# Performance work log

Measured on AMD Instinct MI355X. Metric: run time of the kernel, lower is better.

The kernel has to match this reference:

```python
import jax, jax.numpy as jnp
import numpy as np

D_MODEL = 1024
NUM_HEADS = 16
HEAD_DIM = D_MODEL // NUM_HEADS
SEQ_LEN = 4096
BATCH = 1
ROPE_THETA = 10000.0


def apply_rope(x, theta):
    # x: [B, H, S, D], interleaved pair rotation (x_{2i}, x_{2i+1})
    D = x.shape[-1]
    S = x.shape[-2]
    pos = jnp.arange(S, dtype=jnp.float32)
    inv_freq = theta ** (-jnp.arange(0, D, 2, dtype=jnp.float32) / D)  # [D/2]
    ang = pos[:, None] * inv_freq[None, :]  # [S, D/2]
    cos = jnp.cos(ang).astype(x.dtype)
    sin = jnp.sin(ang).astype(x.dtype)
    x1 = x[..., 0::2]
    x2 = x[..., 1::2]
    r1 = x1 * cos - x2 * sin
    r2 = x1 * sin + x2 * cos
    return jnp.stack([r1, r2], axis=-1).reshape(x.shape)


def setup_inputs() -> dict:
    key = jax.random.key(0)
    ks = jax.random.split(key, 5)
    s = 1.0 / np.sqrt(D_MODEL)
    return {
        "x": jax.random.normal(ks[0], (BATCH, SEQ_LEN, D_MODEL), jnp.float32),
        "Wq": jax.random.normal(ks[1], (D_MODEL, D_MODEL), jnp.float32) * s,
        "Wk": jax.random.normal(ks[2], (D_MODEL, D_MODEL), jnp.float32) * s,
        "Wv": jax.random.normal(ks[3], (D_MODEL, D_MODEL), jnp.float32) * s,
        "Wo": jax.random.normal(ks[4], (D_MODEL, D_MODEL), jnp.float32) * s,
    }


def reference(x, Wq, Wk, Wv, Wo):
    B, S, _ = x.shape
    # bias-free linear: y = x @ W.T
    def proj(W):
        y = jnp.einsum('bsd,ed->bse', x, W)
        return y.reshape(B, S, NUM_HEADS, HEAD_DIM).transpose(0, 2, 1, 3)  # [B,H,S,hd]
    q = apply_rope(proj(Wq), ROPE_THETA)
    k = apply_rope(proj(Wk), ROPE_THETA)
    v = proj(Wv)
    scale = 1.0 / jnp.sqrt(jnp.asarray(HEAD_DIM, dtype=x.dtype))
    scores = jnp.einsum('bhqd,bhkd->bhqk', q, k) * scale  # [B,H,S,S]
    causal = jnp.tril(jnp.ones((S, S), dtype=bool))
    scores = jnp.where(causal, scores, jnp.asarray(-jnp.inf, dtype=scores.dtype))
    attn = jax.nn.softmax(scores, axis=-1)
    out = jnp.einsum('bhqk,bhkd->bhqd', attn, v)
    out = out.transpose(0, 2, 1, 3).reshape(B, S, D_MODEL)
    return jnp.einsum('bsd,ed->bse', out, Wo)
```

## Files before the change

### kernel.cpp

```cpp
#include <hip/hip_runtime.h>
#include <math.h>

#define SEQ 4096
#define DM  1024
#define NH  16

typedef __attribute__((ext_vector_type(8))) short bf16x8;
typedef __attribute__((ext_vector_type(4))) float f32x4;
typedef __attribute__((ext_vector_type(16))) float f32x16;
typedef __attribute__((ext_vector_type(4))) unsigned int u32x4;

#define QSCALE 0.18033688011112042f
#define SMAX 16.0f

__device__ __forceinline__ unsigned short f2bf(float f){
  unsigned int u = __float_as_uint(f);
  u += 0x7fffu + ((u >> 16) & 1u);
  return (unsigned short)(u >> 16);
}

__device__ __forceinline__ unsigned int cvtpk(float lo, float hi){
  unsigned int r;
  asm("v_cvt_pk_bf16_f32 %0, %1, %2" : "=v"(r) : "v"(lo), "v"(hi));
  return r;
}

__device__ __forceinline__ void gload_lds16(const void* g, void* l){
  __builtin_amdgcn_global_load_lds(
      (const __attribute__((address_space(1))) unsigned int*)g,
      (__attribute__((address_space(3))) unsigned int*)l,
      16, 0, 0);
}

__global__ __launch_bounds__(256) void f2bf_kernel(const float* __restrict__ src,
                                                   unsigned short* __restrict__ dst, int n4){
  int i = blockIdx.x * 256 + threadIdx.x;
  int stride = gridDim.x * 256;
  for (; i < n4; i += stride){
    float4 v = ((const float4*)src)[i];
    ushort4 o; o.x = f2bf(v.x); o.y = f2bf(v.y); o.z = f2bf(v.z); o.w = f2bf(v.w);
    ((ushort4*)dst)[i] = o;
  }
}

__global__ __launch_bounds__(256) void wf2bf_kernel(const float* __restrict__ a, const float* __restrict__ b,
                                                    const float* __restrict__ c, const float* __restrict__ d,
                                                    unsigned short* __restrict__ oa, unsigned short* __restrict__ ob,
                                                    unsigned short* __restrict__ oc, unsigned short* __restrict__ od,
                                                    int n4){
  const int sel = blockIdx.y;
  const float* src = (sel == 0) ? a : (sel == 1) ? b : (sel == 2) ? c : d;
  unsigned short* dst = (sel == 0) ? oa : (sel == 1) ? ob : (sel == 2) ? oc : od;
  int i = blockIdx.x * 256 + threadIdx.x;
  int stride = gridDim.x * 256;
  for (; i < n4; i += stride){
    float4 v = ((const float4*)src)[i];
    ushort4 o; o.x = f2bf(v.x); o.y = f2bf(v.y); o.z = f2bf(v.z); o.w = f2bf(v.w);
    ((ushort4*)dst)[i] = o;
  }
}

__global__ __launch_bounds__(256) void rope_tab_kernel(float2* __restrict__ tab){
  int i = blockIdx.x * 256 + threadIdx.x;
  int s = i >> 5, f = i & 31;
  double inv = exp2(-(double)f * (13.287712379549449 / 32.0));
  double a = (double)s * inv;
  const double twopi = 6.283185307179586476;
  a -= twopi * floor(a / twopi);
  float af = (float)a;
  tab[i] = make_float2(cosf(af), sinf(af));
}

__global__ __launch_bounds__(256) void qkv_gemm(const unsigned short* __restrict__ A,
                                                const unsigned short* __restrict__ Wq,
                                                const unsigned short* __restrict__ Wk,
                                                const unsigned short* __restrict__ Wv,
                                                unsigned short* __restrict__ Qo,
                                                unsigned short* __restrict__ Ko,
                                                unsigned short* __restrict__ Vto,
                                                const float2* __restrict__ rope)
{
  __shared__ unsigned short At[128 * 32];
  __shared__ unsigned short Bt[128 * 32];
  const int sel = blockIdx.x >> 3;
  const unsigned short* B = (sel == 0) ? Wq : (sel == 1) ? Wk : Wv;
  const int K = DM;
  const int t = threadIdx.x;
  const int lane = t & 63, w = t >> 6;
  const int lg = lane >> 4, lr = lane & 15;
  const int wr = w >> 1, wc = w & 1;
  const int m0 = blockIdx.y * 128, n0 = (blockIdx.x & 7) * 128;

  f32x4 acc[4][4];
  #pragma unroll
  for (int mi = 0; mi < 4; mi++)
    #pragma unroll
    for (int nj = 0; nj < 4; nj++)
      acc[mi][nj] = (f32x4){0.f, 0.f, 0.f, 0.f};

  for (int k0 = 0; k0 < K; k0 += 32){
    __syncthreads();
    {
      int idx = t;
      gload_lds16(&A[(size_t)(m0 + (idx >> 2)) * K + k0 + (idx & 3) * 8], &At[idx * 8]);
      gload_lds16(&B[(size_t)(n0 + (idx >> 2)) * K + k0 + (idx & 3) * 8], &Bt[idx * 8]);
      idx = t + 256;
      gload_lds16(&A[(size_t)(m0 + (idx >> 2)) * K + k0 + (idx & 3) * 8], &At[idx * 8]);
      gload_lds16(&B[(size_t)(n0 + (idx >> 2)) * K + k0 + (idx & 3) * 8], &Bt[idx * 8]);
    }
    __syncthreads();
    bf16x8 af[4], bfr[4];
    #pragma unroll
    for (int mi = 0; mi < 4; mi++)
      af[mi] = *(const bf16x8*)&At[(wr * 64 + mi * 16 + lr) * 32 + lg * 8];
    #pragma unroll
    for (int nj = 0; nj < 4; nj++)
      bfr[nj] = *(const bf16x8*)&Bt[(wc * 64 + nj * 16 + lr) * 32 + lg * 8];
    #pragma unroll
    for (int mi = 0; mi < 4; mi++)
      #pragma unroll
      for (int nj = 0; nj < 4; nj++)
        acc[mi][nj] = __builtin_amdgcn_mfma_f32_16x16x32_bf16(af[mi], bfr[nj], acc[mi][nj], 0, 0, 0);
  }

  #pragma unroll
  for (int mi = 0; mi < 4; mi++){
    #pragma unroll
    for (int nj = 0; nj < 4; nj++){
      f32x4 v = acc[mi][nj];
      int col  = n0 + wc * 64 + nj * 16 + lr;
      int row0 = m0 + wr * 64 + mi * 16 + lg * 4;
      if (sel == 0){
        #pragma unroll
        for (int j = 0; j < 4; j++){
          float val = v[j];
          float oth = __shfl_xor(val, 1);
          int row = row0 + j;
          int i = (col & 63) >> 1;
          float2 cs = rope[row * 32 + i];
          float res = ((col & 1) == 0) ? (val * cs.x - oth * cs.y)
                                       : (oth * cs.y + val * cs.x);
          Qo[(size_t)row * DM + col] = f2bf(res * QSCALE);
        }
      } else if (sel == 1){
        const int hh = col >> 6, d = col & 63;
        #pragma unroll
        for (int j = 0; j < 4; j++){
          float val = v[j];
          float oth = __shfl_xor(val, 1);
          int row = row0 + j;
          int i = d >> 1;
          float2 cs = rope[row * 32 + i];
          float res = ((d & 1) == 0) ? (val * cs.x - oth * cs.y)
                                     : (oth * cs.y + val * cs.x);
          size_t idx = ((size_t)((hh * 128 + (row >> 5)) * 8 + (d >> 3))) * 256
                       + (row & 31) * 8 + (d & 7);
          Ko[idx] = f2bf(res);
        }
      } else {
        const int hh = col >> 6, d = col & 63;
        ushort4 pkv; pkv.x = f2bf(v[0]); pkv.y = f2bf(v[1]); pkv.z = f2bf(v[2]); pkv.w = f2bf(v[3]);
        size_t idx = ((size_t)(((hh * 2 + (d >> 5)) * 64 + (row0 >> 6)) * 8 + ((row0 >> 3) & 7))) * 256
                     + (d & 31) * 8 + (row0 & 7);
        *(ushort4*)&Vto[idx] = pkv;
      }
    }
  }
}

__global__ __launch_bounds__(256) void gemm_out(const unsigned short* __restrict__ A,
                                                const unsigned short* __restrict__ B,
                                                float* __restrict__ C)
{
  __shared__ unsigned short At[128 * 32];
  __shared__ unsigned short Bt[128 * 32];
  const int K = DM;
  const int t = threadIdx.x;
  const int lane = t & 63, w = t >> 6;
  const int lg = lane >> 4, lr = lane & 15;
  const int wr = w >> 1, wc = w & 1;
  const int m0 = blockIdx.y * 128, n0 = blockIdx.x * 128;

  f32x4 acc[4][4];
  #pragma unroll
  for (int mi = 0; mi < 4; mi++)
    #pragma unroll
    for (int nj = 0; nj < 4; nj++)
      acc[mi][nj] = (f32x4){0.f, 0.f, 0.f, 0.f};

  for (int k0 = 0; k0 < K; k0 += 32){
    __syncthreads();
    {
      int idx = t;
      gload_lds16(&A[(size_t)(m0 + (idx >> 2)) * K + k0 + (idx & 3) * 8], &At[idx * 8]);
      gload_lds16(&B[(size_t)(n0 + (idx >> 2)) * K + k0 + (idx & 3) * 8], &Bt[idx * 8]);
      idx = t + 256;
      gload_lds16(&A[(size_t)(m0 + (idx >> 2)) * K + k0 + (idx & 3) * 8], &At[idx * 8]);
      gload_lds16(&B[(size_t)(n0 + (idx >> 2)) * K + k0 + (idx & 3) * 8], &Bt[idx * 8]);
    }
    __syncthreads();
    bf16x8 af[4], bfr[4];
    #pragma unroll
    for (int mi = 0; mi < 4; mi++)
      af[mi] = *(const bf16x8*)&At[(wr * 64 + mi * 16 + lr) * 32 + lg * 8];
    #pragma unroll
    for (int nj = 0; nj < 4; nj++)
      bfr[nj] = *(const bf16x8*)&Bt[(wc * 64 + nj * 16 + lr) * 32 + lg * 8];
    #pragma unroll
    for (int mi = 0; mi < 4; mi++)
      #pragma unroll
      for (int nj = 0; nj < 4; nj++)
        acc[mi][nj] = __builtin_amdgcn_mfma_f32_16x16x32_bf16(af[mi], bfr[nj], acc[mi][nj], 0, 0, 0);
  }

  #pragma unroll
  for (int mi = 0; mi < 4; mi++)
    #pragma unroll
    for (int nj = 0; nj < 4; nj++){
      f32x4 v = acc[mi][nj];
      int col  = n0 + wc * 64 + nj * 16 + lr;
      int row0 = m0 + wr * 64 + mi * 16 + lg * 4;
      #pragma unroll
      for (int j = 0; j < 4; j++)
        C[(size_t)(row0 + j) * DM + col] = v[j];
    }
}

__global__ __launch_bounds__(256, 4) void attn5_kernel(const unsigned short* __restrict__ Qb,
                                                       const unsigned short* __restrict__ Kp,
                                                       const unsigned short* __restrict__ Vp,
                                                       unsigned short* __restrict__ AO)
{
  __shared__ float oS[3][16][2][64];
  __shared__ float lS[3][32];

  const int h = blockIdx.x;
  const int qi = (int)gridDim.y - 1 - (int)blockIdx.y;
  const int q0 = qi * 32;
  const int t = threadIdx.x, w = t >> 6, lane = t & 63;
  const int ql = lane & 31, hi = lane >> 5;
  const int qrow = q0 + ql;

  const int nkt = (qi >> 1) + 1;

  bf16x8 qf[4];
  #pragma unroll
  for (int ds = 0; ds < 4; ds++)
    qf[ds] = *(const bf16x8*)&Qb[(size_t)qrow * DM + h * 64 + ds * 16 + hi * 8];

  f32x16 oacc[2];
  #pragma unroll
  for (int d = 0; d < 2; d++)
    #pragma unroll
    for (int r = 0; r < 16; r++) oacc[d][r] = 0.f;
  float lrun = 0.f;

  const bf16x8* Kf = (const bf16x8*)Kp + (size_t)h * 128 * 8 * 32;
  const bf16x8* Vf = (const bf16x8*)Vp + (size_t)h * 2 * 64 * 8 * 32;

  for (int kt = w; kt < nkt; kt += 4){
    const int k0 = kt << 6;
    const bool diag = (kt == nkt - 1);
    float p[32];

    __builtin_amdgcn_s_setprio(1);
    #pragma unroll
    for (int st = 0; st < 2; st++){
      bf16x8 kf[4];
      #pragma unroll
      for (int ds = 0; ds < 4; ds++)
        kf[ds] = Kf[(size_t)((kt * 2 + st) * 8 + ds * 2 + hi) * 32 + ql];
      f32x16 s;
      #pragma unroll
      for (int r = 0; r < 16; r++) s[r] = 0.f;
      #pragma unroll
      for (int ds = 0; ds < 4; ds++)
        s = __builtin_amdgcn_mfma_f32_32x32x16_bf16(kf[ds], qf[ds], s, 0, 0, 0);
      if (diag){
        #pragma unroll
        for (int r = 0; r < 16; r++){
          int key = k0 + st * 32 + (r & 3) + 8 * (r >> 2) + 4 * hi;
          p[st * 16 + r] = (key > qrow) ? -INFINITY : s[r];
        }
      } else {
        #pragma unroll
        for (int r = 0; r < 16; r++) p[st * 16 + r] = s[r];
      }
    }
    __builtin_amdgcn_s_setprio(0);

    float ts0 = 0.f, ts1 = 0.f, ts2 = 0.f, ts3 = 0.f;
    #pragma unroll
    for (int i = 0; i < 32; i += 4){
      p[i]     = __builtin_amdgcn_exp2f(p[i]     - SMAX); ts0 += p[i];
      p[i + 1] = __builtin_amdgcn_exp2f(p[i + 1] - SMAX); ts1 += p[i + 1];
      p[i + 2] = __builtin_amdgcn_exp2f(p[i + 2] - SMAX); ts2 += p[i + 2];
      p[i + 3] = __builtin_amdgcn_exp2f(p[i + 3] - SMAX); ts3 += p[i + 3];
    }
    float ts = (ts0 + ts1) + (ts2 + ts3);
    ts += __shfl_xor(ts, 32);
    lrun += ts;

    u32x4 pfr[4];
    #pragma unroll
    for (int ks = 0; ks < 4; ks++){
      int b = ks * 8;
      unsigned int a  = cvtpk(p[b + 0], p[b + 1]);
      unsigned int c  = cvtpk(p[b + 2], p[b + 3]);
      unsigned int bb = cvtpk(p[b + 4], p[b + 5]);
      unsigned int d  = cvtpk(p[b + 6], p[b + 7]);
      unsigned int sa = (unsigned int)__shfl_xor((int)a, 32);
      unsigned int sc = (unsigned int)__shfl_xor((int)c, 32);
      unsigned int sb = (unsigned int)__shfl_xor((int)bb, 32);
      unsigned int sd = (unsigned int)__shfl_xor((int)d, 32);
      pfr[ks][0] = hi ? sb : a;
      pfr[ks][1] = hi ? sd : c;
      pfr[ks][2] = hi ? bb : sa;
      pfr[ks][3] = hi ? d  : sc;
    }

    __builtin_amdgcn_s_setprio(1);
    #pragma unroll
    for (int dcol = 0; dcol < 2; dcol++){
      bf16x8 vf[4];
      #pragma unroll
      for (int ks = 0; ks < 4; ks++)
        vf[ks] = Vf[(size_t)((dcol * 64 + kt) * 8 + ks * 2 + hi) * 32 + ql];
      #pragma unroll
      for (int ks = 0; ks < 4; ks++){
        union { u32x4 u; bf16x8 v; } pf; pf.u = pfr[ks];
        oacc[dcol] = __builtin_amdgcn_mfma_f32_32x32x16_bf16(pf.v, vf[ks], oacc[dcol], 0, 0, 0);
      }
    }
    __builtin_amdgcn_s_setprio(0);
  }

  if (w > 0){
    if (hi == 0) lS[w - 1][ql] = lrun;
    #pragma unroll
    for (int r = 0; r < 16; r++)
      #pragma unroll
      for (int dcol = 0; dcol < 2; dcol++)
        oS[w - 1][r][hi][dcol * 32 + ql] = oacc[dcol][r];
  }
  __syncthreads();
  if (w == 0){
    float lstar = lrun + lS[0][ql] + lS[1][ql] + lS[2][ql];
    float rl = 1.f / lstar;
    #pragma unroll
    for (int r = 0; r < 16; r++){
      int rowloc = (r & 3) + 8 * (r >> 2) + 4 * hi;
      float rr = __shfl(rl, rowloc);
      int row = q0 + rowloc;
      #pragma unroll
      for (int dcol = 0; dcol < 2; dcol++){
        int dd = dcol * 32 + ql;
        float o = oacc[dcol][r] + oS[0][r][hi][dd] + oS[1][r][hi][dd] + oS[2][r][hi][dd];
        AO[(size_t)row * DM + h * 64 + dd] = f2bf(o * rr);
      }
    }
  }
}

extern "C" void kernel_launch(void* const* d_in, const int* in_sizes, int n_in,
                              void* d_out, int out_size, void* d_ws, size_t ws_size,
                              hipStream_t stream)
{
  const float* x  = (const float*)d_in[0];
  const float* Wq = (const float*)d_in[1];
  const float* Wk = (const float*)d_in[2];
  const float* Wv = (const float*)d_in[3];
  const float* Wo = (const float*)d_in[4];

  char* ws = (char*)d_ws;
  unsigned short* xb  = (unsigned short*)ws; ws += (size_t)SEQ * DM * 2;
  unsigned short* wqb = (unsigned short*)ws; ws += (size_t)DM * DM * 2;
  unsigned short* wkb = (unsigned short*)ws; ws += (size_t)DM * DM * 2;
  unsigned short* wvb = (unsigned short*)ws; ws += (size_t)DM * DM * 2;
  unsigned short* wob = (unsigned short*)ws; ws += (size_t)DM * DM * 2;
  unsigned short* Qb  = (unsigned short*)ws; ws += (size_t)SEQ * DM * 2;
  unsigned short* Kpr = (unsigned short*)ws; ws += (size_t)SEQ * DM * 2;
  unsigned short* Vpr = (unsigned short*)ws; ws += (size_t)DM * SEQ * 2;
  unsigned short* AO  = (unsigned short*)ws; ws += (size_t)SEQ * DM * 2;
  float2* ropetab     = (float2*)ws;         ws += (size_t)SEQ * 32 * sizeof(float2);

  f2bf_kernel<<<1024, 256, 0, stream>>>(x, xb, SEQ * DM / 4);
  wf2bf_kernel<<<dim3(128, 4), 256, 0, stream>>>(Wq, Wk, Wv, Wo, wqb, wkb, wvb, wob, DM * DM / 4);
  rope_tab_kernel<<<SEQ * 32 / 256, 256, 0, stream>>>(ropetab);

  qkv_gemm<<<dim3(24, 32), 256, 0, stream>>>(xb, wqb, wkb, wvb, Qb, Kpr, Vpr, ropetab);

  attn5_kernel<<<dim3(NH, SEQ / 32), 256, 0, stream>>>(Qb, Kpr, Vpr, AO);

  gemm_out<<<dim3(8, 32), 256, 0, stream>>>(AO, wob, (float*)d_out);
}
```

Before: 154.3 us.

## Use K=64 swizzled LDS tiles in GEMMs; fold softmax offset into MFMA init; pack attention partials

Both projection GEMMs now stage 64-wide K tiles, halving the number of barrier pairs per K loop. They store rows in LDS with an XOR swizzle of 16-byte chunks to avoid bank conflicts on the fragment reads. In attention, the fixed softmax offset is folded into the MFMA accumulator initial value, which removes a subtraction per exponent. The cross-wave partial outputs are exchanged as packed bf16 pairs instead of fp32, halving LDS traffic for the final reduction at some precision cost.

```diff
diff --git a/kernel.cpp b/kernel.cpp
--- a/kernel.cpp
+++ b/kernel.cpp
@@ -80,8 +80,8 @@
                                                 unsigned short* __restrict__ Vto,
                                                 const float2* __restrict__ rope)
 {
-  __shared__ unsigned short At[128 * 32];
-  __shared__ unsigned short Bt[128 * 32];
+  __shared__ unsigned short At[128 * 64];
+  __shared__ unsigned short Bt[128 * 64];
   const int sel = blockIdx.x >> 3;
   const unsigned short* B = (sel == 0) ? Wq : (sel == 1) ? Wk : Wv;
   const int K = DM;
@@ -98,29 +98,38 @@
     for (int nj = 0; nj < 4; nj++)
       acc[mi][nj] = (f32x4){0.f, 0.f, 0.f, 0.f};
 
-  for (int k0 = 0; k0 < K; k0 += 32){
+  for (int k0 = 0; k0 < K; k0 += 64){
     __syncthreads();
-    {
-      int idx = t;
-      gload_lds16(&A[(size_t)(m0 + (idx >> 2)) * K + k0 + (idx & 3) * 8], &At[idx * 8]);
-      gload_lds16(&B[(size_t)(n0 + (idx >> 2)) * K + k0 + (idx & 3) * 8], &Bt[idx * 8]);
-      idx = t + 256;
-      gload_lds16(&A[(size_t)(m0 + (idx >> 2)) * K + k0 + (idx & 3) * 8], &At[idx * 8]);
-      gload_lds16(&B[(size_t)(n0 + (idx >> 2)) * K + k0 + (idx & 3) * 8], &Bt[idx * 8]);
+    #pragma unroll
+    for (int r = 0; r < 4; r++){
+      int idx = r * 256 + t, row = idx >> 3, ch = idx & 7, cs = ch ^ (row & 7);
+      gload_lds16(&A[(size_t)(m0 + row) * K + k0 + cs * 8], &At[idx * 8]);
+    }
+    #pragma unroll
+    for (int r = 0; r < 4; r++){
+      int idx = r * 256 + t, row = idx >> 3, ch = idx & 7, cs = ch ^ (row & 7);
+      gload_lds16(&B[(size_t)(n0 + row) * K + k0 + cs * 8], &Bt[idx * 8]);
     }
     __syncthreads();
-    bf16x8 af[4], bfr[4];
-    #pragma unroll
-    for (int mi = 0; mi < 4; mi++)
-      af[mi] = *(const bf16x8*)&At[(wr * 64 + mi * 16 + lr) * 32 + lg * 8];
-    #pragma unroll
-    for (int nj = 0; nj < 4; nj++)
-      bfr[nj] = *(const bf16x8*)&Bt[(wc * 64 + nj * 16 + lr) * 32 + lg * 8];
-    #pragma unroll
-    for (int mi = 0; mi < 4; mi++)
-      #pragma unroll
-      for (int nj = 0; nj < 4; nj++)
-        acc[mi][nj] = __builtin_amdgcn_mfma_f32_16x16x32_bf16(af[mi], bfr[nj], acc[mi][nj], 0, 0, 0);
+    #pragma unroll
+    for (int kk = 0; kk < 2; kk++){
+      bf16x8 af[4], bfr[4];
+      #pragma unroll
+      for (int mi = 0; mi < 4; mi++){
+        int row = wr * 64 + mi * 16 + lr;
+        af[mi] = *(const bf16x8*)&At[row * 64 + (((kk * 4 + lg) ^ (row & 7)) << 3)];
+      }
+      #pragma unroll
+      for (int nj = 0; nj < 4; nj++){
+        int row = wc * 64 + nj * 16 + lr;
+        bfr[nj] = *(const bf16x8*)&Bt[row * 64 + (((kk * 4 + lg) ^ (row & 7)) << 3)];
+      }
+      #pragma unroll
+      for (int mi = 0; mi < 4; mi++)
+        #pragma unroll
+        for (int nj = 0; nj < 4; nj++)
+          acc[mi][nj] = __builtin_amdgcn_mfma_f32_16x16x32_bf16(af[mi], bfr[nj], acc[mi][nj], 0, 0, 0);
+    }
   }
 
   #pragma unroll
@@ -172,8 +181,8 @@
                                                 const unsigned short* __restrict__ B,
                                                 float* __restrict__ C)
 {
-  __shared__ unsigned short At[128 * 32];
-  __shared__ unsigned short Bt[128 * 32];
+  __shared__ unsigned short At[128 * 64];
+  __shared__ unsigned short Bt[128 * 64];
   const int K = DM;
   const int t = threadIdx.x;
   const int lane = t & 63, w = t >> 6;
@@ -188,29 +197,38 @@
     for (int nj = 0; nj < 4; nj++)
       acc[mi][nj] = (f32x4){0.f, 0.f, 0.f, 0.f};
 
-  for (int k0 = 0; k0 < K; k0 += 32){
+  for (int k0 = 0; k0 < K; k0 += 64){
     __syncthreads();
-    {
-      int idx = t;
-      gload_lds16(&A[(size_t)(m0 + (idx >> 2)) * K + k0 + (idx & 3) * 8], &At[idx * 8]);
-      gload_lds16(&B[(size_t)(n0 + (idx >> 2)) * K + k0 + (idx & 3) * 8], &Bt[idx * 8]);
-      idx = t + 256;
-      gload_lds16(&A[(size_t)(m0 + (idx >> 2)) * K + k0 + (idx & 3) * 8], &At[idx * 8]);
-      gload_lds16(&B[(size_t)(n0 + (idx >> 2)) * K + k0 + (idx & 3) * 8], &Bt[idx * 8]);
+    #pragma unroll
+    for (int r = 0; r < 4; r++){
+      int idx = r * 256 + t, row = idx >> 3, ch = idx & 7, cs = ch ^ (row & 7);
+      gload_lds16(&A[(size_t)(m0 + row) * K + k0 + cs * 8], &At[idx * 8]);
+    }
+    #pragma unroll
+    for (int r = 0; r < 4; r++){
+      int idx = r * 256 + t, row = idx >> 3, ch = idx & 7, cs = ch ^ (row & 7);
+      gload_lds16(&B[(size_t)(n0 + row) * K + k0 + cs * 8], &Bt[idx * 8]);
     }
     __syncthreads();
-    bf16x8 af[4], bfr[4];
-    #pragma unroll
-    for (int mi = 0; mi < 4; mi++)
-      af[mi] = *(const bf16x8*)&At[(wr * 64 + mi * 16 + lr) * 32 + lg * 8];
-    #pragma unroll
-    for (int nj = 0; nj < 4; nj++)
-      bfr[nj] = *(const bf16x8*)&Bt[(wc * 64 + nj * 16 + lr) * 32 + lg * 8];
-    #pragma unroll
-    for (int mi = 0; mi < 4; mi++)
-      #pragma unroll
-      for (int nj = 0; nj < 4; nj++)
-        acc[mi][nj] = __builtin_amdgcn_mfma_f32_16x16x32_bf16(af[mi], bfr[nj], acc[mi][nj], 0, 0, 0);
+    #pragma unroll
+    for (int kk = 0; kk < 2; kk++){
+      bf16x8 af[4], bfr[4];
+      #pragma unroll
+      for (int mi = 0; mi < 4; mi++){
+        int row = wr * 64 + mi * 16 + lr;
+        af[mi] = *(const bf16x8*)&At[row * 64 + (((kk * 4 + lg) ^ (row & 7)) << 3)];
+      }
+      #pragma unroll
+      for (int nj = 0; nj < 4; nj++){
+        int row = wc * 64 + nj * 16 + lr;
+        bfr[nj] = *(const bf16x8*)&Bt[row * 64 + (((kk * 4 + lg) ^ (row & 7)) << 3)];
+      }
+      #pragma unroll
+      for (int mi = 0; mi < 4; mi++)
+        #pragma unroll
+        for (int nj = 0; nj < 4; nj++)
+          acc[mi][nj] = __builtin_amdgcn_mfma_f32_16x16x32_bf16(af[mi], bfr[nj], acc[mi][nj], 0, 0, 0);
+    }
   }
 
   #pragma unroll
@@ -226,12 +244,12 @@
     }
 }
 
-__global__ __launch_bounds__(256, 4) void attn5_kernel(const unsigned short* __restrict__ Qb,
+__global__ __launch_bounds__(256, 4) void attn6_kernel(const unsigned short* __restrict__ Qb,
                                                        const unsigned short* __restrict__ Kp,
                                                        const unsigned short* __restrict__ Vp,
                                                        unsigned short* __restrict__ AO)
 {
-  __shared__ float oS[3][16][2][64];
+  __shared__ unsigned int oS[3][16][2][32];
   __shared__ float lS[3][32];
 
   const int h = blockIdx.x;
@@ -272,7 +290,7 @@
         kf[ds] = Kf[(size_t)((kt * 2 + st) * 8 + ds * 2 + hi) * 32 + ql];
       f32x16 s;
       #pragma unroll
-      for (int r = 0; r < 16; r++) s[r] = 0.f;
+      for (int r = 0; r < 16; r++) s[r] = -SMAX;
       #pragma unroll
       for (int ds = 0; ds < 4; ds++)
         s = __builtin_amdgcn_mfma_f32_32x32x16_bf16(kf[ds], qf[ds], s, 0, 0, 0);
@@ -292,10 +310,10 @@
     float ts0 = 0.f, ts1 = 0.f, ts2 = 0.f, ts3 = 0.f;
     #pragma unroll
     for (int i = 0; i < 32; i += 4){
-      p[i]     = __builtin_amdgcn_exp2f(p[i]     - SMAX); ts0 += p[i];
-      p[i + 1] = __builtin_amdgcn_exp2f(p[i + 1] - SMAX); ts1 += p[i + 1];
-      p[i + 2] = __builtin_amdgcn_exp2f(p[i + 2] - SMAX); ts2 += p[i + 2];
-      p[i + 3] = __builtin_amdgcn_exp2f(p[i + 3] - SMAX); ts3 += p[i + 3];
+      p[i]     = __builtin_amdgcn_exp2f(p[i]);     ts0 += p[i];
+      p[i + 1] = __builtin_amdgcn_exp2f(p[i + 1]); ts1 += p[i + 1];
+      p[i + 2] = __builtin_amdgcn_exp2f(p[i + 2]); ts2 += p[i + 2];
+      p[i + 3] = __builtin_amdgcn_exp2f(p[i + 3]); ts3 += p[i + 3];
     }
     float ts = (ts0 + ts1) + (ts2 + ts3);
     ts += __shfl_xor(ts, 32);
@@ -339,9 +357,7 @@
     if (hi == 0) lS[w - 1][ql] = lrun;
     #pragma unroll
     for (int r = 0; r < 16; r++)
-      #pragma unroll
-      for (int dcol = 0; dcol < 2; dcol++)
-        oS[w - 1][r][hi][dcol * 32 + ql] = oacc[dcol][r];
+      oS[w - 1][r][hi][ql] = cvtpk(oacc[0][r], oacc[1][r]);
   }
   __syncthreads();
   if (w == 0){
@@ -352,12 +368,15 @@
       int rowloc = (r & 3) + 8 * (r >> 2) + 4 * hi;
       float rr = __shfl(rl, rowloc);
       int row = q0 + rowloc;
-      #pragma unroll
-      for (int dcol = 0; dcol < 2; dcol++){
-        int dd = dcol * 32 + ql;
-        float o = oacc[dcol][r] + oS[0][r][hi][dd] + oS[1][r][hi][dd] + oS[2][r][hi][dd];
-        AO[(size_t)row * DM + h * 64 + dd] = f2bf(o * rr);
-      }
+      float o0 = oacc[0][r], o1 = oacc[1][r];
+      #pragma unroll
+      for (int j = 0; j < 3; j++){
+        unsigned int u = oS[j][r][hi][ql];
+        o0 += __uint_as_float(u << 16);
+        o1 += __uint_as_float(u & 0xffff0000u);
+      }
+      AO[(size_t)row * DM + h * 64 + ql]      = f2bf(o0 * rr);
+      AO[(size_t)row * DM + h * 64 + 32 + ql] = f2bf(o1 * rr);
     }
   }
 }
@@ -390,7 +409,7 @@
 
   qkv_gemm<<<dim3(24, 32), 256, 0, stream>>>(xb, wqb, wkb, wvb, Qb, Kpr, Vpr, ropetab);
 
-  attn5_kernel<<<dim3(NH, SEQ / 32), 256, 0, stream>>>(Qb, Kpr, Vpr, AO);
+  attn6_kernel<<<dim3(NH, SEQ / 32), 256, 0, stream>>>(Qb, Kpr, Vpr, AO);
 
   gemm_out<<<dim3(8, 32), 256, 0, stream>>>(AO, wob, (float*)d_out);
 }
```

New measurement: 170.6 us. 1.11x slower.
